# Optimization experiments

Measured on AMD Instinct MI355X. Metric: run time of the kernel, lower is better.

Reference implementation:

```python
import jax, jax.numpy as jnp
import numpy as np

N_NODES = 50000


def gcn_conv(x, W, b, src, dst, n):
    """PyG GCNConv: add self-loops, sym-normalize, linear, scatter-add."""
    loop = jnp.arange(n, dtype=src.dtype)
    s = jnp.concatenate([src, loop])  # [E+N]
    d = jnp.concatenate([dst, loop])
    deg = jax.ops.segment_sum(jnp.ones_like(s, dtype=x.dtype), d, num_segments=n)
    dinv = jnp.where(deg > 0, jax.lax.rsqrt(deg), 0.0)  # deg^-1/2
    norm = dinv[s] * dinv[d]  # [E+N]
    h = x @ W  # [N, out] dense GEMM first (in >= out)
    msg = h[s] * norm[:, None]  # gather + scale
    out = jax.ops.segment_sum(msg, d, num_segments=n)  # scatter-add
    return out + b


def setup_inputs() -> dict:
    key = jax.random.key(0)
    k1, k2, k3, k4, k5, k6, k7, k8 = jax.random.split(key, 8)
    in_c, hid_c, out_c = 512, 128, 64
    n, e, l = N_NODES, 800000, 100000
    x = jax.random.normal(k1, (n, in_c), dtype=jnp.float32)
    edge_index = jax.random.randint(k2, (2, e), 0, n, dtype=jnp.int64)
    edge_label_index = jax.random.randint(k3, (2, l), 0, n, dtype=jnp.int64)
    # Glorot-ish init for weights, zeros for biases (PyG default bias=zeros)
    W1 = jax.random.normal(k4, (in_c, hid_c), dtype=jnp.float32) / np.sqrt(in_c)
    b1 = jnp.zeros((hid_c,), dtype=jnp.float32)
    W2 = jax.random.normal(k5, (hid_c, out_c), dtype=jnp.float32) / np.sqrt(hid_c)
    b2 = jnp.zeros((out_c,), dtype=jnp.float32)
    return {"x": x, "edge_index": edge_index, "edge_label_index": edge_label_index,
            "W1": W1, "b1": b1, "W2": W2, "b2": b2}


def reference(x, edge_index, edge_label_index, W1, b1, W2, b2):
    n = x.shape[0]
    src, dst = edge_index[0], edge_index[1]
    z = jax.nn.relu(gcn_conv(x, W1, b1, src, dst, n))
    z = gcn_conv(z, W2, b2, src, dst, n)
    es, ed = edge_label_index[0], edge_label_index[1]
    return jnp.sum(z[es] * z[ed], axis=-1).reshape(-1)
```

## Files before the change

kernel.cpp:

```cpp
#include <hip/hip_runtime.h>

#define IN_C  512
#define HID_C 128
#define OUT_C 64

using short8 = __attribute__((ext_vector_type(8))) short;
using floatx4 = __attribute__((ext_vector_type(4))) float;

__device__ inline unsigned short f2bf(float f) {
    unsigned u = __builtin_bit_cast(unsigned, f);
    u += 0x7FFFu + ((u >> 16) & 1u);
    return (unsigned short)(u >> 16);
}
__device__ inline float bf2f(unsigned short h) {
    unsigned u = ((unsigned)h) << 16;
    return __builtin_bit_cast(float, u);
}
__device__ inline unsigned short f2h(float f) {
    _Float16 h = (_Float16)f;
    return __builtin_bit_cast(unsigned short, h);
}
__device__ inline float h2f(unsigned v) {
    return (float)__builtin_bit_cast(_Float16, (unsigned short)v);
}
__device__ inline unsigned packh2(float a, float b) {
    return (unsigned)f2h(a) | ((unsigned)f2h(b) << 16);
}

__global__ void k_zero_int(int* __restrict__ p, int n) {
    int i = blockIdx.x * blockDim.x + threadIdx.x;
    if (i < n) p[i] = 0;
}

__global__ void k_count(const int* __restrict__ dst, int* __restrict__ cnt, int e) {
    int i = blockIdx.x * blockDim.x + threadIdx.x;
    if (i < e) atomicAdd(&cnt[dst[i]], 1);
}

__global__ void k_blocksum_dinv(const int* __restrict__ cnt, int* __restrict__ bsum,
                                float* __restrict__ dinv, int n) {
    __shared__ int sdata[256];
    int t = threadIdx.x;
    int i = blockIdx.x * 256 + t;
    int c = (i < n) ? cnt[i] : 0;
    if (i < n) dinv[i] = rsqrtf(1.0f + (float)c);
    sdata[t] = c;
    __syncthreads();
    for (int s = 128; s > 0; s >>= 1) {
        if (t < s) sdata[t] += sdata[t + s];
        __syncthreads();
    }
    if (t == 0) bsum[blockIdx.x] = sdata[0];
}

__global__ void k_scanpartials(int* __restrict__ bsum, int nb) {
    __shared__ int sdata[256];
    int t = threadIdx.x;
    int orig = (t < nb) ? bsum[t] : 0;
    sdata[t] = orig;
    __syncthreads();
    for (int off = 1; off < 256; off <<= 1) {
        int v = (t >= off) ? sdata[t - off] : 0;
        __syncthreads();
        sdata[t] += v;
        __syncthreads();
    }
    if (t < nb) bsum[t] = sdata[t] - orig;
}

__global__ void k_scanfinal(const int* __restrict__ cnt, const int* __restrict__ bsum_ex,
                            int* __restrict__ row_ptr, int n, int e_total) {
    __shared__ int sdata[256];
    int t = threadIdx.x;
    int i = blockIdx.x * 256 + t;
    int orig = (i < n) ? cnt[i] : 0;
    sdata[t] = orig;
    __syncthreads();
    for (int off = 1; off < 256; off <<= 1) {
        int v = (t >= off) ? sdata[t - off] : 0;
        __syncthreads();
        sdata[t] += v;
        __syncthreads();
    }
    if (i < n) row_ptr[i] = sdata[t] - orig + bsum_ex[blockIdx.x];
    if (i == 0) row_ptr[n] = e_total;
}

__global__ void k_fill(const int* __restrict__ src, const int* __restrict__ dst,
                       const int* __restrict__ row_ptr, int* __restrict__ cnt,
                       int* __restrict__ col, int e) {
    int i = blockIdx.x * blockDim.x + threadIdx.x;
    if (i < e) {
        int d = dst[i];
        int pos = atomicSub(&cnt[d], 1) - 1;
        col[row_ptr[d] + pos] = src[i];
    }
}

__global__ void k_prep_w2(const float* __restrict__ W1, unsigned short* __restrict__ hi1,
                          unsigned short* __restrict__ lo1, const float* __restrict__ W2,
                          unsigned short* __restrict__ hi2, unsigned short* __restrict__ lo2) {
    int i = blockIdx.x * blockDim.x + threadIdx.x;
    if (i < IN_C * HID_C) {
        int k = i / HID_C, n = i % HID_C;
        float v = W1[i];
        unsigned short h = f2bf(v);
        hi1[(long)n * IN_C + k] = h;
        lo1[(long)n * IN_C + k] = f2bf(v - bf2f(h));
    } else if (i < IN_C * HID_C + HID_C * OUT_C) {
        int j = i - IN_C * HID_C;
        int k = j / OUT_C, n = j % OUT_C;
        float v = W2[j];
        unsigned short h = f2bf(v);
        hi2[(long)n * HID_C + k] = h;
        lo2[(long)n * HID_C + k] = f2bf(v - bf2f(h));
    }
}

__global__ __launch_bounds__(512) void k_gemm_mfma8(
    const float* __restrict__ A, const unsigned short* __restrict__ Bt_hi,
    const unsigned short* __restrict__ Bt_lo, const float* __restrict__ dinv,
    unsigned short* __restrict__ Hs, int M) {
    constexpr int K = IN_C;
    constexpr int N = HID_C;
    constexpr int LDA = 72;
    constexpr int NT = K / 64;
    __shared__ __align__(16) unsigned short As_hi[2][64 * LDA];
    __shared__ __align__(16) unsigned short As_lo[2][64 * LDA];

    const int tid = threadIdx.x;
    const int w = tid >> 6;
    const int lane = tid & 63;
    const int m = lane & 15;
    const int quad = lane >> 4;
    const int m0 = blockIdx.x * 64;

    const int srow = tid >> 3;
    const int skk = (tid & 7) << 2;

    floatx4 acc[4];
#pragma unroll
    for (int mi = 0; mi < 4; ++mi) acc[mi] = (floatx4){0.f, 0.f, 0.f, 0.f};

    float4 pf[2];
    auto issueA = [&](int t0) {
        int gm = m0 + srow;
        pf[0] = make_float4(0.f, 0.f, 0.f, 0.f);
        pf[1] = make_float4(0.f, 0.f, 0.f, 0.f);
        if (gm < M) {
            pf[0] = *(const float4*)&A[(long)gm * K + t0 * 64 + skk];
            pf[1] = *(const float4*)&A[(long)gm * K + t0 * 64 + skk + 32];
        }
    };
    auto convA = [&](int b) {
#pragma unroll
        for (int i = 0; i < 2; ++i) {
            ushort4 h, l;
            h.x = f2bf(pf[i].x); l.x = f2bf(pf[i].x - bf2f(h.x));
            h.y = f2bf(pf[i].y); l.y = f2bf(pf[i].y - bf2f(h.y));
            h.z = f2bf(pf[i].z); l.z = f2bf(pf[i].z - bf2f(h.z));
            h.w = f2bf(pf[i].w); l.w = f2bf(pf[i].w - bf2f(h.w));
            int off = srow * LDA + skk + 32 * i;
            *(ushort4*)&As_hi[b][off] = h;
            *(ushort4*)&As_lo[b][off] = l;
        }
    };

    issueA(0);
    convA(0);

    for (int t = 0; t < NT; ++t) {
        __syncthreads();
        const int buf = t & 1;
        if (t + 1 < NT) issueA(t + 1);
#pragma unroll
        for (int s = 0; s < 2; ++s) {
            short8 ah[4], al[4];
#pragma unroll
            for (int mi = 0; mi < 4; ++mi) {
                int off = (mi * 16 + m) * LDA + s * 32 + quad * 8;
                ah[mi] = *(const short8*)&As_hi[buf][off];
                al[mi] = *(const short8*)&As_lo[buf][off];
            }
            int n = w * 16 + m;
            long boff = (long)n * K + t * 64 + s * 32 + quad * 8;
            short8 bh = *(const short8*)&Bt_hi[boff];
            short8 bl = *(const short8*)&Bt_lo[boff];
#pragma unroll
            for (int mi = 0; mi < 4; ++mi) {
                acc[mi] = __builtin_amdgcn_mfma_f32_16x16x32_bf16(ah[mi], bh, acc[mi], 0, 0, 0);
                acc[mi] = __builtin_amdgcn_mfma_f32_16x16x32_bf16(ah[mi], bl, acc[mi], 0, 0, 0);
                acc[mi] = __builtin_amdgcn_mfma_f32_16x16x32_bf16(al[mi], bh, acc[mi], 0, 0, 0);
            }
        }
        if (t + 1 < NT) convA(buf ^ 1);
    }

#pragma unroll
    for (int mi = 0; mi < 4; ++mi) {
#pragma unroll
        for (int r = 0; r < 4; ++r) {
            int row = m0 + mi * 16 + quad * 4 + r;
            if (row < M) {
                int n = w * 16 + m;
                Hs[(long)row * N + n] = f2h(acc[mi][r] * dinv[row]);
            }
        }
    }
}

template <int K, int NPW, bool AH, typename AT>
__global__ __launch_bounds__(256) void k_gemm_mfma(
    const AT* __restrict__ A, const unsigned short* __restrict__ Bt_hi,
    const unsigned short* __restrict__ Bt_lo, const float* __restrict__ dinv,
    unsigned short* __restrict__ Hs, int M) {
    constexpr int N = 64 * NPW;
    constexpr int LDA = 72;
    constexpr int NT = K / 64;
    __shared__ __align__(16) unsigned short As_hi[2][64 * LDA];
    __shared__ __align__(16) unsigned short As_lo[2][64 * LDA];

    const int tid = threadIdx.x;
    const int w = tid >> 6;
    const int lane = tid & 63;
    const int m = lane & 15;
    const int quad = lane >> 4;
    const int m0 = blockIdx.x * 64;

    const int srow = tid >> 4;
    const int skk = (tid & 15) << 2;

    floatx4 acc[4][NPW];
#pragma unroll
    for (int mi = 0; mi < 4; ++mi)
#pragma unroll
        for (int ni = 0; ni < NPW; ++ni) acc[mi][ni] = (floatx4){0.f, 0.f, 0.f, 0.f};

    float4 pf[4];
    auto issueA = [&](int t0) {
#pragma unroll
        for (int i = 0; i < 4; ++i) {
            int gm = m0 + srow + 16 * i;
            pf[i] = make_float4(0.f, 0.f, 0.f, 0.f);
            if (gm < M) {
                if constexpr (AH) {
                    ushort4 r = *(const ushort4*)&A[(long)gm * K + t0 * 64 + skk];
                    pf[i] = make_float4(h2f(r.x), h2f(r.y), h2f(r.z), h2f(r.w));
                } else {
                    pf[i] = *(const float4*)&A[(long)gm * K + t0 * 64 + skk];
                }
            }
        }
    };
    auto convA = [&](int b) {
#pragma unroll
        for (int i = 0; i < 4; ++i) {
            ushort4 h, l;
            h.x = f2bf(pf[i].x); l.x = f2bf(pf[i].x - bf2f(h.x));
            h.y = f2bf(pf[i].y); l.y = f2bf(pf[i].y - bf2f(h.y));
            h.z = f2bf(pf[i].z); l.z = f2bf(pf[i].z - bf2f(h.z));
            h.w = f2bf(pf[i].w); l.w = f2bf(pf[i].w - bf2f(h.w));
            int off = (srow + 16 * i) * LDA + skk;
            *(ushort4*)&As_hi[b][off] = h;
            *(ushort4*)&As_lo[b][off] = l;
        }
    };

    issueA(0);
    convA(0);

    for (int t = 0; t < NT; ++t) {
        __syncthreads();
        const int buf = t & 1;
        if (t + 1 < NT) issueA(t + 1);
#pragma unroll
        for (int s = 0; s < 2; ++s) {
            short8 ah[4], al[4];
#pragma unroll
            for (int mi = 0; mi < 4; ++mi) {
                int off = (mi * 16 + m) * LDA + s * 32 + quad * 8;
                ah[mi] = *(const short8*)&As_hi[buf][off];
                al[mi] = *(const short8*)&As_lo[buf][off];
            }
#pragma unroll
            for (int ni = 0; ni < NPW; ++ni) {
                int n = (w * NPW + ni) * 16 + m;
                long boff = (long)n * K + t * 64 + s * 32 + quad * 8;
                short8 bh = *(const short8*)&Bt_hi[boff];
                short8 bl = *(const short8*)&Bt_lo[boff];
#pragma unroll
                for (int mi = 0; mi < 4; ++mi) {
                    acc[mi][ni] = __builtin_amdgcn_mfma_f32_16x16x32_bf16(ah[mi], bh, acc[mi][ni], 0, 0, 0);
                    acc[mi][ni] = __builtin_amdgcn_mfma_f32_16x16x32_bf16(ah[mi], bl, acc[mi][ni], 0, 0, 0);
                    acc[mi][ni] = __builtin_amdgcn_mfma_f32_16x16x32_bf16(al[mi], bh, acc[mi][ni], 0, 0, 0);
                }
            }
        }
        if (t + 1 < NT) convA(buf ^ 1);
    }

#pragma unroll
    for (int mi = 0; mi < 4; ++mi) {
#pragma unroll
        for (int r = 0; r < 4; ++r) {
            int row = m0 + mi * 16 + quad * 4 + r;
            if (row < M) {
                float dv = dinv[row];
#pragma unroll
                for (int ni = 0; ni < NPW; ++ni) {
                    int n = (w * NPW + ni) * 16 + m;
                    Hs[(long)row * N + n] = f2h(acc[mi][ni][r] * dv);
                }
            }
        }
    }
}

__global__ __launch_bounds__(256) void k_agg1(
    const unsigned short* __restrict__ h, const int* __restrict__ row_ptr,
    const int* __restrict__ col, const float* __restrict__ dinv,
    const float* __restrict__ bias, unsigned short* __restrict__ z, int n) {
    int node = blockIdx.x * 4 + (threadIdx.x >> 6);
    node = __builtin_amdgcn_readfirstlane(node);
    if (node >= n) return;
    int lane = threadIdx.x & 63;
    int q = lane >> 4, li = lane & 15;
    const uint4* hp = (const uint4*)h;
    float acc[8] = {0.f, 0.f, 0.f, 0.f, 0.f, 0.f, 0.f, 0.f};
    auto addrow = [&](uint4 v) {
        acc[0] += h2f(v.x); acc[1] += h2f(v.x >> 16);
        acc[2] += h2f(v.y); acc[3] += h2f(v.y >> 16);
        acc[4] += h2f(v.z); acc[5] += h2f(v.z >> 16);
        acc[6] += h2f(v.w); acc[7] += h2f(v.w >> 16);
    };
    if (q == 0) addrow(hp[(long)node * 16 + li]);
    int rs = row_ptr[node], re = row_ptr[node + 1];
    int j = rs + q;
    for (; j + 12 < re; j += 16) {
        int s0 = col[j], s1 = col[j + 4], s2 = col[j + 8], s3 = col[j + 12];
        uint4 v0 = hp[(long)s0 * 16 + li];
        uint4 v1 = hp[(long)s1 * 16 + li];
        uint4 v2 = hp[(long)s2 * 16 + li];
        uint4 v3 = hp[(long)s3 * 16 + li];
        addrow(v0); addrow(v1); addrow(v2); addrow(v3);
    }
    for (; j + 4 < re; j += 8) {
        int s0 = col[j], s1 = col[j + 4];
        uint4 v0 = hp[(long)s0 * 16 + li];
        uint4 v1 = hp[(long)s1 * 16 + li];
        addrow(v0); addrow(v1);
    }
    for (; j < re; j += 4) addrow(hp[(long)col[j] * 16 + li]);
#pragma unroll
    for (int k = 0; k < 8; ++k) {
        acc[k] += __shfl_xor(acc[k], 16);
        acc[k] += __shfl_xor(acc[k], 32);
    }
    if (q == 0) {
        float dv = dinv[node];
        const float4* bp = (const float4*)bias;
        float4 b0 = bp[li * 2], b1 = bp[li * 2 + 1];
        uint4 o;
        o.x = packh2(fmaxf(fmaf(acc[0], dv, b0.x), 0.f), fmaxf(fmaf(acc[1], dv, b0.y), 0.f));
        o.y = packh2(fmaxf(fmaf(acc[2], dv, b0.z), 0.f), fmaxf(fmaf(acc[3], dv, b0.w), 0.f));
        o.z = packh2(fmaxf(fmaf(acc[4], dv, b1.x), 0.f), fmaxf(fmaf(acc[5], dv, b1.y), 0.f));
        o.w = packh2(fmaxf(fmaf(acc[6], dv, b1.z), 0.f), fmaxf(fmaf(acc[7], dv, b1.w), 0.f));
        ((uint4*)z)[(long)node * 16 + li] = o;
    }
}

__global__ __launch_bounds__(256) void k_agg2(
    const unsigned short* __restrict__ h, const int* __restrict__ row_ptr,
    const int* __restrict__ col, const float* __restrict__ dinv,
    const float* __restrict__ bias, float* __restrict__ z, int n) {
    int node = blockIdx.x * 4 + (threadIdx.x >> 6);
    node = __builtin_amdgcn_readfirstlane(node);
    if (node >= n) return;
    int lane = threadIdx.x & 63;
    int q = lane >> 4, li = lane & 15;
    const uint2* hp = (const uint2*)h;
    float acc[4] = {0.f, 0.f, 0.f, 0.f};
    auto addrow = [&](uint2 v) {
        acc[0] += h2f(v.x); acc[1] += h2f(v.x >> 16);
        acc[2] += h2f(v.y); acc[3] += h2f(v.y >> 16);
    };
    if (q == 0) addrow(hp[(long)node * 16 + li]);
    int rs = row_ptr[node], re = row_ptr[node + 1];
    int j = rs + q;
    for (; j + 12 < re; j += 16) {
        int s0 = col[j], s1 = col[j + 4], s2 = col[j + 8], s3 = col[j + 12];
        uint2 v0 = hp[(long)s0 * 16 + li];
        uint2 v1 = hp[(long)s1 * 16 + li];
        uint2 v2 = hp[(long)s2 * 16 + li];
        uint2 v3 = hp[(long)s3 * 16 + li];
        addrow(v0); addrow(v1); addrow(v2); addrow(v3);
    }
    for (; j + 4 < re; j += 8) {
        int s0 = col[j], s1 = col[j + 4];
        uint2 v0 = hp[(long)s0 * 16 + li];
        uint2 v1 = hp[(long)s1 * 16 + li];
        addrow(v0); addrow(v1);
    }
    for (; j < re; j += 4) addrow(hp[(long)col[j] * 16 + li]);
#pragma unroll
    for (int k = 0; k < 4; ++k) {
        acc[k] += __shfl_xor(acc[k], 16);
        acc[k] += __shfl_xor(acc[k], 32);
    }
    if (q == 0) {
        float dv = dinv[node];
        float4 b = ((const float4*)bias)[li];
        float4 o;
        o.x = fmaf(acc[0], dv, b.x);
        o.y = fmaf(acc[1], dv, b.y);
        o.z = fmaf(acc[2], dv, b.z);
        o.w = fmaf(acc[3], dv, b.w);
        ((float4*)z)[(long)node * 16 + li] = o;
    }
}

__global__ void k_dot(const float* __restrict__ z2, const int* __restrict__ es,
                      const int* __restrict__ ed, float* __restrict__ out, int L) {
    int gid = blockIdx.x * blockDim.x + threadIdx.x;
    int wid = gid >> 6;
    int lane = threadIdx.x & 63;
    int q = lane >> 4, li = lane & 15;
    int e = wid * 4 + q;
    if (e >= L) return;
    int a = es[e], b = ed[e];
    const float4* zp = (const float4*)z2;
    float4 za = zp[(long)a * 16 + li];
    float4 zb = zp[(long)b * 16 + li];
    float v = za.x * zb.x + za.y * zb.y + za.z * zb.z + za.w * zb.w;
#pragma unroll
    for (int off = 8; off > 0; off >>= 1) v += __shfl_xor(v, off);
    if (li == 0) out[e] = v;
}

extern "C" void kernel_launch(void* const* d_in, const int* in_sizes, int n_in,
                              void* d_out, int out_size, void* d_ws, size_t ws_size,
                              hipStream_t stream) {
    const float* x = (const float*)d_in[0];
    const int* ei = (const int*)d_in[1];
    const int* eli = (const int*)d_in[2];
    const float* W1 = (const float*)d_in[3];
    const float* b1 = (const float*)d_in[4];
    const float* W2 = (const float*)d_in[5];
    const float* b2 = (const float*)d_in[6];
    float* out = (float*)d_out;

    const int N = in_sizes[0] / IN_C;
    const int E = in_sizes[1] / 2;
    const int L = in_sizes[2] / 2;
    const int* src = ei;
    const int* dst = ei + E;
    const int* es = eli;
    const int* ed = eli + L;

    const int Npad = (N + 63) & ~63;
    const int Epad = (E + 3) & ~3;

    int* cnt = (int*)d_ws;
    int* row_ptr = cnt + Npad;
    int* bsum = row_ptr + Npad + 64;
    int* col = bsum + 256;
    float* dinv = (float*)(col + Epad);
    unsigned short* h1s = (unsigned short*)(dinv + Npad);
    unsigned short* z1 = h1s + (long)N * HID_C;
    unsigned short* h2s = h1s;
    float* z2 = (float*)(z1 + (long)N * HID_C);
    unsigned short* wt1_hi = (unsigned short*)(z2 + (long)N * OUT_C);
    unsigned short* wt1_lo = wt1_hi + IN_C * HID_C;
    unsigned short* wt2_hi = wt1_lo + IN_C * HID_C;
    unsigned short* wt2_lo = wt2_hi + HID_C * OUT_C;

    const int TPB = 256;
    const int nb = (N + 255) / 256;

    const int PW = IN_C * HID_C + HID_C * OUT_C;
    k_prep_w2<<<(PW + TPB - 1) / TPB, TPB, 0, stream>>>(W1, wt1_hi, wt1_lo, W2, wt2_hi, wt2_lo);

    k_zero_int<<<(Npad + TPB - 1) / TPB, TPB, 0, stream>>>(cnt, Npad);
    k_count<<<(E + TPB - 1) / TPB, TPB, 0, stream>>>(dst, cnt, E);
    k_blocksum_dinv<<<nb, 256, 0, stream>>>(cnt, bsum, dinv, N);
    k_scanpartials<<<1, 256, 0, stream>>>(bsum, nb);
    k_scanfinal<<<nb, 256, 0, stream>>>(cnt, bsum, row_ptr, N, E);
    k_fill<<<(E + TPB - 1) / TPB, TPB, 0, stream>>>(src, dst, row_ptr, cnt, col, E);

    k_gemm_mfma8<<<(N + 63) / 64, 512, 0, stream>>>(x, wt1_hi, wt1_lo, dinv, h1s, N);
    k_agg1<<<(N + 3) / 4, 256, 0, stream>>>(h1s, row_ptr, col, dinv, b1, z1, N);

    k_gemm_mfma<HID_C, 1, true><<<(N + 63) / 64, 256, 0, stream>>>(z1, wt2_hi, wt2_lo, dinv, h2s, N);
    k_agg2<<<(N + 3) / 4, 256, 0, stream>>>(h2s, row_ptr, col, dinv, b2, z2, N);

    k_dot<<<((long)((L + 3) / 4) * 64 + TPB - 1) / TPB, TPB, 0, stream>>>(z2, es, ed, out, L);
}
```

Baseline: 357.9 us.

## Fuse zeroing into weight prep, pre-scale CSR indices, widen layer-2 GEMM

Merges the count-buffer zeroing into the weight-prep kernel to drop one launch. CSR column entries now store src<<4, so the aggregation kernels skip a multiply per gathered row. The layer-2 GEMM is replaced with a 512-thread variant that splits the 64x64 tile across 8 waves (2 M-subtiles each) for more parallelism per block. The changes are small and independent; the GEMM change trades per-wave work for occupancy.

```diff
diff --git a/kernel.cpp b/kernel.cpp
--- a/kernel.cpp
+++ b/kernel.cpp
@@ -27,79 +27,10 @@
     return (unsigned)f2h(a) | ((unsigned)f2h(b) << 16);
 }
 
-__global__ void k_zero_int(int* __restrict__ p, int n) {
-    int i = blockIdx.x * blockDim.x + threadIdx.x;
-    if (i < n) p[i] = 0;
-}
-
-__global__ void k_count(const int* __restrict__ dst, int* __restrict__ cnt, int e) {
-    int i = blockIdx.x * blockDim.x + threadIdx.x;
-    if (i < e) atomicAdd(&cnt[dst[i]], 1);
-}
-
-__global__ void k_blocksum_dinv(const int* __restrict__ cnt, int* __restrict__ bsum,
-                                float* __restrict__ dinv, int n) {
-    __shared__ int sdata[256];
-    int t = threadIdx.x;
-    int i = blockIdx.x * 256 + t;
-    int c = (i < n) ? cnt[i] : 0;
-    if (i < n) dinv[i] = rsqrtf(1.0f + (float)c);
-    sdata[t] = c;
-    __syncthreads();
-    for (int s = 128; s > 0; s >>= 1) {
-        if (t < s) sdata[t] += sdata[t + s];
-        __syncthreads();
-    }
-    if (t == 0) bsum[blockIdx.x] = sdata[0];
-}
-
-__global__ void k_scanpartials(int* __restrict__ bsum, int nb) {
-    __shared__ int sdata[256];
-    int t = threadIdx.x;
-    int orig = (t < nb) ? bsum[t] : 0;
-    sdata[t] = orig;
-    __syncthreads();
-    for (int off = 1; off < 256; off <<= 1) {
-        int v = (t >= off) ? sdata[t - off] : 0;
-        __syncthreads();
-        sdata[t] += v;
-        __syncthreads();
-    }
-    if (t < nb) bsum[t] = sdata[t] - orig;
-}
-
-__global__ void k_scanfinal(const int* __restrict__ cnt, const int* __restrict__ bsum_ex,
-                            int* __restrict__ row_ptr, int n, int e_total) {
-    __shared__ int sdata[256];
-    int t = threadIdx.x;
-    int i = blockIdx.x * 256 + t;
-    int orig = (i < n) ? cnt[i] : 0;
-    sdata[t] = orig;
-    __syncthreads();
-    for (int off = 1; off < 256; off <<= 1) {
-        int v = (t >= off) ? sdata[t - off] : 0;
-        __syncthreads();
-        sdata[t] += v;
-        __syncthreads();
-    }
-    if (i < n) row_ptr[i] = sdata[t] - orig + bsum_ex[blockIdx.x];
-    if (i == 0) row_ptr[n] = e_total;
-}
-
-__global__ void k_fill(const int* __restrict__ src, const int* __restrict__ dst,
-                       const int* __restrict__ row_ptr, int* __restrict__ cnt,
-                       int* __restrict__ col, int e) {
-    int i = blockIdx.x * blockDim.x + threadIdx.x;
-    if (i < e) {
-        int d = dst[i];
-        int pos = atomicSub(&cnt[d], 1) - 1;
-        col[row_ptr[d] + pos] = src[i];
-    }
-}
-
-__global__ void k_prep_w2(const float* __restrict__ W1, unsigned short* __restrict__ hi1,
-                          unsigned short* __restrict__ lo1, const float* __restrict__ W2,
-                          unsigned short* __restrict__ hi2, unsigned short* __restrict__ lo2) {
+__global__ void k_prep_zero(const float* __restrict__ W1, unsigned short* __restrict__ hi1,
+                            unsigned short* __restrict__ lo1, const float* __restrict__ W2,
+                            unsigned short* __restrict__ hi2, unsigned short* __restrict__ lo2,
+                            int* __restrict__ cnt, int npad) {
     int i = blockIdx.x * blockDim.x + threadIdx.x;
     if (i < IN_C * HID_C) {
         int k = i / HID_C, n = i % HID_C;
@@ -114,6 +45,74 @@
         unsigned short h = f2bf(v);
         hi2[(long)n * HID_C + k] = h;
         lo2[(long)n * HID_C + k] = f2bf(v - bf2f(h));
+    } else {
+        int j = i - (IN_C * HID_C + HID_C * OUT_C);
+        if (j < npad) cnt[j] = 0;
+    }
+}
+
+__global__ void k_count(const int* __restrict__ dst, int* __restrict__ cnt, int e) {
+    int i = blockIdx.x * blockDim.x + threadIdx.x;
+    if (i < e) atomicAdd(&cnt[dst[i]], 1);
+}
+
+__global__ void k_blocksum_dinv(const int* __restrict__ cnt, int* __restrict__ bsum,
+                                float* __restrict__ dinv, int n) {
+    __shared__ int sdata[256];
+    int t = threadIdx.x;
+    int i = blockIdx.x * 256 + t;
+    int c = (i < n) ? cnt[i] : 0;
+    if (i < n) dinv[i] = rsqrtf(1.0f + (float)c);
+    sdata[t] = c;
+    __syncthreads();
+    for (int s = 128; s > 0; s >>= 1) {
+        if (t < s) sdata[t] += sdata[t + s];
+        __syncthreads();
+    }
+    if (t == 0) bsum[blockIdx.x] = sdata[0];
+}
+
+__global__ void k_scanpartials(int* __restrict__ bsum, int nb) {
+    __shared__ int sdata[256];
+    int t = threadIdx.x;
+    int orig = (t < nb) ? bsum[t] : 0;
+    sdata[t] = orig;
+    __syncthreads();
+    for (int off = 1; off < 256; off <<= 1) {
+        int v = (t >= off) ? sdata[t - off] : 0;
+        __syncthreads();
+        sdata[t] += v;
+        __syncthreads();
+    }
+    if (t < nb) bsum[t] = sdata[t] - orig;
+}
+
+__global__ void k_scanfinal(const int* __restrict__ cnt, const int* __restrict__ bsum_ex,
+                            int* __restrict__ row_ptr, int n, int e_total) {
+    __shared__ int sdata[256];
+    int t = threadIdx.x;
+    int i = blockIdx.x * 256 + t;
+    int orig = (i < n) ? cnt[i] : 0;
+    sdata[t] = orig;
+    __syncthreads();
+    for (int off = 1; off < 256; off <<= 1) {
+        int v = (t >= off) ? sdata[t - off] : 0;
+        __syncthreads();
+        sdata[t] += v;
+        __syncthreads();
+    }
+    if (i < n) row_ptr[i] = sdata[t] - orig + bsum_ex[blockIdx.x];
+    if (i == 0) row_ptr[n] = e_total;
+}
+
+__global__ void k_fill(const int* __restrict__ src, const int* __restrict__ dst,
+                       const int* __restrict__ row_ptr, int* __restrict__ cnt,
+                       int* __restrict__ col, int e) {
+    int i = blockIdx.x * blockDim.x + threadIdx.x;
+    if (i < e) {
+        int d = dst[i];
+        int pos = atomicSub(&cnt[d], 1) - 1;
+        col[row_ptr[d] + pos] = src[i] << 4;
     }
 }
 
@@ -209,12 +208,12 @@
     }
 }
 
-template <int K, int NPW, bool AH, typename AT>
-__global__ __launch_bounds__(256) void k_gemm_mfma(
-    const AT* __restrict__ A, const unsigned short* __restrict__ Bt_hi,
+__global__ __launch_bounds__(512) void k_gemm_mfma8_l2(
+    const unsigned short* __restrict__ A, const unsigned short* __restrict__ Bt_hi,
     const unsigned short* __restrict__ Bt_lo, const float* __restrict__ dinv,
     unsigned short* __restrict__ Hs, int M) {
-    constexpr int N = 64 * NPW;
+    constexpr int K = HID_C;
+    constexpr int N = OUT_C;
     constexpr int LDA = 72;
     constexpr int NT = K / 64;
     __shared__ __align__(16) unsigned short As_hi[2][64 * LDA];
@@ -222,45 +221,41 @@
 
     const int tid = threadIdx.x;
     const int w = tid >> 6;
+    const int wm = w >> 2;
+    const int wn = w & 3;
     const int lane = tid & 63;
     const int m = lane & 15;
     const int quad = lane >> 4;
     const int m0 = blockIdx.x * 64;
 
-    const int srow = tid >> 4;
-    const int skk = (tid & 15) << 2;
-
-    floatx4 acc[4][NPW];
-#pragma unroll
-    for (int mi = 0; mi < 4; ++mi)
-#pragma unroll
-        for (int ni = 0; ni < NPW; ++ni) acc[mi][ni] = (floatx4){0.f, 0.f, 0.f, 0.f};
-
-    float4 pf[4];
+    const int srow = tid >> 3;
+    const int skk = (tid & 7) << 2;
+
+    floatx4 acc[2];
+    acc[0] = (floatx4){0.f, 0.f, 0.f, 0.f};
+    acc[1] = (floatx4){0.f, 0.f, 0.f, 0.f};
+
+    float4 pf[2];
     auto issueA = [&](int t0) {
-#pragma unroll
-        for (int i = 0; i < 4; ++i) {
-            int gm = m0 + srow + 16 * i;
-            pf[i] = make_float4(0.f, 0.f, 0.f, 0.f);
-            if (gm < M) {
-                if constexpr (AH) {
-                    ushort4 r = *(const ushort4*)&A[(long)gm * K + t0 * 64 + skk];
-                    pf[i] = make_float4(h2f(r.x), h2f(r.y), h2f(r.z), h2f(r.w));
-                } else {
-                    pf[i] = *(const float4*)&A[(long)gm * K + t0 * 64 + skk];
-                }
-            }
+        int gm = m0 + srow;
+        pf[0] = make_float4(0.f, 0.f, 0.f, 0.f);
+        pf[1] = make_float4(0.f, 0.f, 0.f, 0.f);
+        if (gm < M) {
+            ushort4 r0 = *(const ushort4*)&A[(long)gm * K + t0 * 64 + skk];
+            ushort4 r1 = *(const ushort4*)&A[(long)gm * K + t0 * 64 + skk + 32];
+            pf[0] = make_float4(h2f(r0.x), h2f(r0.y), h2f(r0.z), h2f(r0.w));
+            pf[1] = make_float4(h2f(r1.x), h2f(r1.y), h2f(r1.z), h2f(r1.w));
         }
     };
     auto convA = [&](int b) {
 #pragma unroll
-        for (int i = 0; i < 4; ++i) {
+        for (int i = 0; i < 2; ++i) {
             ushort4 h, l;
             h.x = f2bf(pf[i].x); l.x = f2bf(pf[i].x - bf2f(h.x));
             h.y = f2bf(pf[i].y); l.y = f2bf(pf[i].y - bf2f(h.y));
             h.z = f2bf(pf[i].z); l.z = f2bf(pf[i].z - bf2f(h.z));
             h.w = f2bf(pf[i].w); l.w = f2bf(pf[i].w - bf2f(h.w));
-            int off = (srow + 16 * i) * LDA + skk;
+            int off = srow * LDA + skk + 32 * i;
             *(ushort4*)&As_hi[b][off] = h;
             *(ushort4*)&As_lo[b][off] = l;
         }
@@ -275,42 +270,35 @@
         if (t + 1 < NT) issueA(t + 1);
 #pragma unroll
         for (int s = 0; s < 2; ++s) {
-            short8 ah[4], al[4];
-#pragma unroll
-            for (int mi = 0; mi < 4; ++mi) {
-                int off = (mi * 16 + m) * LDA + s * 32 + quad * 8;
+            short8 ah[2], al[2];
+#pragma unroll
+            for (int mi = 0; mi < 2; ++mi) {
+                int off = ((wm * 2 + mi) * 16 + m) * LDA + s * 32 + quad * 8;
                 ah[mi] = *(const short8*)&As_hi[buf][off];
                 al[mi] = *(const short8*)&As_lo[buf][off];
             }
-#pragma unroll
-            for (int ni = 0; ni < NPW; ++ni) {
-                int n = (w * NPW + ni) * 16 + m;
-                long boff = (long)n * K + t * 64 + s * 32 + quad * 8;
-                short8 bh = *(const short8*)&Bt_hi[boff];
-                short8 bl = *(const short8*)&Bt_lo[boff];
-#pragma unroll
-                for (int mi = 0; mi < 4; ++mi) {
-                    acc[mi][ni] = __builtin_amdgcn_mfma_f32_16x16x32_bf16(ah[mi], bh, acc[mi][ni], 0, 0, 0);
-                    acc[mi][ni] = __builtin_amdgcn_mfma_f32_16x16x32_bf16(ah[mi], bl, acc[mi][ni], 0, 0, 0);
-                    acc[mi][ni] = __builtin_amdgcn_mfma_f32_16x16x32_bf16(al[mi], bh, acc[mi][ni], 0, 0, 0);
-                }
+            int n = wn * 16 + m;
+            long boff = (long)n * K + t * 64 + s * 32 + quad * 8;
+            short8 bh = *(const short8*)&Bt_hi[boff];
+            short8 bl = *(const short8*)&Bt_lo[boff];
+#pragma unroll
+            for (int mi = 0; mi < 2; ++mi) {
+                acc[mi] = __builtin_amdgcn_mfma_f32_16x16x32_bf16(ah[mi], bh, acc[mi], 0, 0, 0);
+                acc[mi] = __builtin_amdgcn_mfma_f32_16x16x32_bf16(ah[mi], bl, acc[mi], 0, 0, 0);
+                acc[mi] = __builtin_amdgcn_mfma_f32_16x16x32_bf16(al[mi], bh, acc[mi], 0, 0, 0);
             }
         }
         if (t + 1 < NT) convA(buf ^ 1);
     }
 
 #pragma unroll
-    for (int mi = 0; mi < 4; ++mi) {
+    for (int mi = 0; mi < 2; ++mi) {
 #pragma unroll
         for (int r = 0; r < 4; ++r) {
-            int row = m0 + mi * 16 + quad * 4 + r;
+            int row = m0 + (wm * 2 + mi) * 16 + quad * 4 + r;
             if (row < M) {
-                float dv = dinv[row];
-#pragma unroll
-                for (int ni = 0; ni < NPW; ++ni) {
-                    int n = (w * NPW + ni) * 16 + m;
-                    Hs[(long)row * N + n] = f2h(acc[mi][ni][r] * dv);
-                }
+                int n = wn * 16 + m;
+                Hs[(long)row * N + n] = f2h(acc[mi][r] * dinv[row]);
             }
         }
     }
@@ -338,19 +326,19 @@
     int j = rs + q;
     for (; j + 12 < re; j += 16) {
         int s0 = col[j], s1 = col[j + 4], s2 = col[j + 8], s3 = col[j + 12];
-        uint4 v0 = hp[(long)s0 * 16 + li];
-        uint4 v1 = hp[(long)s1 * 16 + li];
-        uint4 v2 = hp[(long)s2 * 16 + li];
-        uint4 v3 = hp[(long)s3 * 16 + li];
+        uint4 v0 = hp[(long)s0 + li];
+        uint4 v1 = hp[(long)s1 + li];
+        uint4 v2 = hp[(long)s2 + li];
+        uint4 v3 = hp[(long)s3 + li];
         addrow(v0); addrow(v1); addrow(v2); addrow(v3);
     }
     for (; j + 4 < re; j += 8) {
         int s0 = col[j], s1 = col[j + 4];
-        uint4 v0 = hp[(long)s0 * 16 + li];
-        uint4 v1 = hp[(long)s1 * 16 + li];
+        uint4 v0 = hp[(long)s0 + li];
+        uint4 v1 = hp[(long)s1 + li];
         addrow(v0); addrow(v1);
     }
-    for (; j < re; j += 4) addrow(hp[(long)col[j] * 16 + li]);
+    for (; j < re; j += 4) addrow(hp[(long)col[j] + li]);
 #pragma unroll
     for (int k = 0; k < 8; ++k) {
         acc[k] += __shfl_xor(acc[k], 16);
@@ -389,19 +377,19 @@
     int j = rs + q;
     for (; j + 12 < re; j += 16) {
         int s0 = col[j], s1 = col[j + 4], s2 = col[j + 8], s3 = col[j + 12];
-        uint2 v0 = hp[(long)s0 * 16 + li];
-        uint2 v1 = hp[(long)s1 * 16 + li];
-        uint2 v2 = hp[(long)s2 * 16 + li];
-        uint2 v3 = hp[(long)s3 * 16 + li];
+        uint2 v0 = hp[(long)s0 + li];
+        uint2 v1 = hp[(long)s1 + li];
+        uint2 v2 = hp[(long)s2 + li];
+        uint2 v3 = hp[(long)s3 + li];
         addrow(v0); addrow(v1); addrow(v2); addrow(v3);
     }
     for (; j + 4 < re; j += 8) {
         int s0 = col[j], s1 = col[j + 4];
-        uint2 v0 = hp[(long)s0 * 16 + li];
-        uint2 v1 = hp[(long)s1 * 16 + li];
+        uint2 v0 = hp[(long)s0 + li];
+        uint2 v1 = hp[(long)s1 + li];
         addrow(v0); addrow(v1);
     }
-    for (; j < re; j += 4) addrow(hp[(long)col[j] * 16 + li]);
+    for (; j < re; j += 4) addrow(hp[(long)col[j] + li]);
 #pragma unroll
     for (int k = 0; k < 4; ++k) {
         acc[k] += __shfl_xor(acc[k], 16);
@@ -477,10 +465,9 @@
     const int TPB = 256;
     const int nb = (N + 255) / 256;
 
-    const int PW = IN_C * HID_C + HID_C * OUT_C;
-    k_prep_w2<<<(PW + TPB - 1) / TPB, TPB, 0, stream>>>(W1, wt1_hi, wt1_lo, W2, wt2_hi, wt2_lo);
-
-    k_zero_int<<<(Npad + TPB - 1) / TPB, TPB, 0, stream>>>(cnt, Npad);
+    const int PW = IN_C * HID_C + HID_C * OUT_C + Npad;
+    k_prep_zero<<<(PW + TPB - 1) / TPB, TPB, 0, stream>>>(W1, wt1_hi, wt1_lo, W2, wt2_hi, wt2_lo, cnt, Npad);
+
     k_count<<<(E + TPB - 1) / TPB, TPB, 0, stream>>>(dst, cnt, E);
     k_blocksum_dinv<<<nb, 256, 0, stream>>>(cnt, bsum, dinv, N);
     k_scanpartials<<<1, 256, 0, stream>>>(bsum, nb);
@@ -490,7 +477,7 @@
     k_gemm_mfma8<<<(N + 63) / 64, 512, 0, stream>>>(x, wt1_hi, wt1_lo, dinv, h1s, N);
     k_agg1<<<(N + 3) / 4, 256, 0, stream>>>(h1s, row_ptr, col, dinv, b1, z1, N);
 
-    k_gemm_mfma<HID_C, 1, true><<<(N + 63) / 64, 256, 0, stream>>>(z1, wt2_hi, wt2_lo, dinv, h2s, N);
+    k_gemm_mfma8_l2<<<(N + 63) / 64, 512, 0, stream>>>(z1, wt2_hi, wt2_lo, dinv, h2s, N);
     k_agg2<<<(N + 3) / 4, 256, 0, stream>>>(h2s, row_ptr, col, dinv, b2, z2, N);
 
     k_dot<<<((long)((L + 3) / 4) * 64 + TPB - 1) / TPB, TPB, 0, stream>>>(z2, es, ed, out, L);
```

Result: no change. 354.4 us (-1.0%).
